# Kernel optimization log

Measured on AMD Instinct MI355X. Metric: run time of the kernel, lower is better.

The kernel has to match this reference:

```python
import jax, jax.numpy as jnp
import numpy as np

N = 50000
E = 800000
D_IN = 128
D_H = 128
D_OUT = 128
G = 64
EPS = 1e-5


def setup_inputs() -> dict:
    key = jax.random.key(0)
    ks = jax.random.split(key, 16)
    s = 0.05
    x = jax.random.normal(ks[0], (N, D_IN), dtype=jnp.float32)
    edge_index = jax.random.randint(ks[1], (2, E), 0, N, dtype=jnp.int64)
    batch = jnp.sort(jax.random.randint(ks[2], (N,), 0, G, dtype=jnp.int64))
    return {
        "x": x,
        "edge_index": edge_index,
        "batch": batch,
        "W1": jax.random.normal(ks[3], (D_IN, D_H), jnp.float32) * s,
        "a_src1": jax.random.normal(ks[4], (D_H,), jnp.float32) * s,
        "a_dst1": jax.random.normal(ks[5], (D_H,), jnp.float32) * s,
        "b1": jnp.zeros((D_H,), jnp.float32),
        "W2": jax.random.normal(ks[6], (D_H, D_H), jnp.float32) * s,
        "a_src2": jax.random.normal(ks[7], (D_H,), jnp.float32) * s,
        "a_dst2": jax.random.normal(ks[8], (D_H,), jnp.float32) * s,
        "b2": jnp.zeros((D_H,), jnp.float32),
        "ln1_g": jnp.ones((D_H,), jnp.float32),
        "ln1_b": jnp.zeros((D_H,), jnp.float32),
        "ln2_g": jnp.ones((D_H,), jnp.float32),
        "ln2_b": jnp.zeros((D_H,), jnp.float32),
        "fc_W": jax.random.normal(ks[9], (D_H, D_OUT), jnp.float32) * s,
        "fc_b": jnp.zeros((D_OUT,), jnp.float32),
        "bn_g": jnp.ones((D_OUT,), jnp.float32),
        "bn_b": jnp.zeros((D_OUT,), jnp.float32),
    }


def gat_conv(x, src, dst, W, a_src, a_dst, b):
    # PyG GATConv, heads=1, concat=False. src=j (message source), dst=i (target).
    h = x @ W                              # [N, C]
    al_s = h @ a_src                       # [N]
    al_d = h @ a_dst                       # [N]
    alpha = jax.nn.leaky_relu(al_s[src] + al_d[dst], 0.2)  # [E']
    m = jax.ops.segment_max(alpha, dst, num_segments=N)    # segment softmax (stable)
    e = jnp.exp(alpha - m[dst])
    z = jax.ops.segment_sum(e, dst, num_segments=N)
    w = e / z[dst]                          # [E']
    out = jax.ops.segment_sum(w[:, None] * h[src], dst, num_segments=N)
    return out + b


def layer_norm(x, g, b):
    mu = jnp.mean(x, axis=-1, keepdims=True)
    var = jnp.mean((x - mu) ** 2, axis=-1, keepdims=True)
    return (x - mu) * jax.lax.rsqrt(var + EPS) * g + b


def reference(x, edge_index, batch, W1, a_src1, a_dst1, b1, W2, a_src2, a_dst2, b2,
              ln1_g, ln1_b, ln2_g, ln2_b, fc_W, fc_b, bn_g, bn_b):
    # add self loops (PyG GATConv default)
    sl = jnp.arange(N, dtype=edge_index.dtype)
    src = jnp.concatenate([edge_index[0], sl])
    dst = jnp.concatenate([edge_index[1], sl])

    h = jax.nn.relu(gat_conv(x, src, dst, W1, a_src1, a_dst1, b1))
    h = layer_norm(h, ln1_g, ln1_b)
    # dropout is identity in eval
    h = gat_conv(h, src, dst, W2, a_src2, a_dst2, b2)
    h = layer_norm(h, ln2_g, ln2_b)
    h = jax.nn.relu(h)

    # global mean pool over graphs
    sums = jax.ops.segment_sum(h, batch, num_segments=G)            # [G, D_H]
    cnts = jax.ops.segment_sum(jnp.ones((N,), h.dtype), batch, num_segments=G)
    pooled = sums / jnp.maximum(cnts, 1.0)[:, None]

    logits = pooled @ fc_W + fc_b                                   # [G, D_OUT]
    # BatchNorm1d (training-mode batch stats, biased variance)
    mu = jnp.mean(logits, axis=0)
    var = jnp.mean((logits - mu) ** 2, axis=0)
    logits = (logits - mu) * jax.lax.rsqrt(var + EPS) * bn_g + bn_b
    return logits
```

## Files before the change

kernel.cpp:

```cpp
#include <hip/hip_runtime.h>
#include <hip/hip_bf16.h>
#include <math.h>

#define N_NODES 50000
#define N_EDGES 800000
#define EN (N_EDGES + N_NODES)
#define D 128
#define G_GRAPHS 64
#define EPS 1e-5f
#define POOL_ROWS_PER_WAVE 64
#define N_TILES 3125
#define LIN_BLOCKS ((N_TILES + 15) / 16)

#define NBUCK 196
#define BCAP 8192
#define EPB 4096
#define BIN_BLOCKS ((EN + EPB - 1) / EPB)

typedef short short8 __attribute__((ext_vector_type(8)));
typedef float f32x4  __attribute__((ext_vector_type(4)));
typedef unsigned short us8 __attribute__((ext_vector_type(8)));

__device__ __forceinline__ float wave_reduce_sum(float v) {
  #pragma unroll
  for (int off = 32; off > 0; off >>= 1) v += __shfl_xor(v, off, 64);
  return v;
}
__device__ __forceinline__ int wave_reduce_sum_i(int v) {
  #pragma unroll
  for (int off = 32; off > 0; off >>= 1) v += __shfl_xor(v, off, 64);
  return v;
}

__device__ __forceinline__ float bf_to_f(unsigned short u) {
  union { unsigned int i; float f; } a;
  a.i = ((unsigned int)u) << 16;
  return a.f;
}
__device__ __forceinline__ unsigned short f_to_bf(float f) {
  union { float f; unsigned int i; } v; v.f = f;
  unsigned int r = v.i + 0x7FFF + ((v.i >> 16) & 1);
  return (unsigned short)(r >> 16);
}


__global__ __launch_bounds__(256) void bin_kernel(
    const int* __restrict__ ei, int* __restrict__ gcnt, uint2* __restrict__ bedges) {
  __shared__ int hist[NBUCK], base[NBUCK], curl[NBUCK];
  int tid = threadIdx.x;
  for (int i = tid; i < NBUCK; i += 256) { hist[i] = 0; curl[i] = 0; }
  __syncthreads();
  int e0 = blockIdx.x * EPB;
  int srcs[16], dsts[16];
  #pragma unroll
  for (int i = 0; i < 16; ++i) {
    int e = e0 + i * 256 + tid;
    int s = -1, d = -1;
    if (e < N_EDGES)   { s = ei[e]; d = ei[N_EDGES + e]; }
    else if (e < EN)   { s = e - N_EDGES; d = s; }
    srcs[i] = s; dsts[i] = d;
    if (d >= 0) atomicAdd(&hist[d >> 8], 1);
  }
  __syncthreads();
  for (int i = tid; i < NBUCK; i += 256)
    base[i] = atomicAdd(&gcnt[i], hist[i]);
  __syncthreads();
  #pragma unroll
  for (int i = 0; i < 16; ++i) {
    int d = dsts[i];
    if (d < 0) continue;
    int b = d >> 8;
    int pos = base[b] + atomicAdd(&curl[b], 1);
    if (pos < BCAP) bedges[(size_t)b * BCAP + pos] = make_uint2((unsigned)srcs[i], (unsigned)d);
  }
}

__global__ __launch_bounds__(256) void bucket_csr_kernel(
    const uint2* __restrict__ bedges, const int* __restrict__ gcnt,
    int* __restrict__ offs, int* __restrict__ esrc, float* __restrict__ sums) {
  __shared__ int hist[256], pex[256], curl[256], scanbuf[256];
  __shared__ int wsum[4];
  int b = blockIdx.x, t = threadIdx.x;
  if (b == 0) {
    for (int i = t; i < G_GRAPHS * D; i += 256) sums[i] = 0.f;
    if (t == 0) offs[N_NODES] = EN;
  }
  int pv = (t < b) ? gcnt[t] : 0;
  int v = wave_reduce_sum_i(pv);
  if ((t & 63) == 0) wsum[t >> 6] = v;
  hist[t] = 0; curl[t] = 0;
  __syncthreads();
  int gb = wsum[0] + wsum[1] + wsum[2] + wsum[3];
  int m = gcnt[b]; if (m > BCAP) m = BCAP;
  int node0 = b << 8;
  const uint2* be = bedges + (size_t)b * BCAP;
  for (int k = t; k < m; k += 256) atomicAdd(&hist[be[k].y & 255], 1);
  __syncthreads();
  int h = hist[t];
  scanbuf[t] = h;
  __syncthreads();
  #pragma unroll
  for (int off = 1; off < 256; off <<= 1) {
    int add = (t >= off) ? scanbuf[t - off] : 0;
    __syncthreads();
    scanbuf[t] += add;
    __syncthreads();
  }
  pex[t] = scanbuf[t] - h;
  int node = node0 + t;
  if (node < N_NODES) offs[node] = gb + pex[t];
  __syncthreads();
  for (int k = t; k < m; k += 256) {
    uint2 e = be[k];
    int n = e.y & 255;
    int r = atomicAdd(&curl[n], 1);
    esrc[gb + pex[n] + r] = (int)e.x;
  }
}


__global__ __launch_bounds__(1024) void linear_mfma_kernel(
    const unsigned short* __restrict__ Xb, const float* __restrict__ Xf,
    const float* __restrict__ W,
    const float* __restrict__ a_s, const float* __restrict__ a_d,
    unsigned short* __restrict__ Hb, float* __restrict__ AS, float* __restrict__ AD) {
  __shared__ unsigned short Wl[D * D];
  int tid = threadIdx.x;
  #pragma unroll
  for (int it = 0; it < 16; ++it) {
    int flat = it * 1024 + tid;
    int r = flat >> 7, col = flat & 127;
    int c = r >> 5, rem = r & 31, quad = rem >> 3, j = rem & 7;
    int t = col >> 4, l = quad * 16 + (col & 15);
    Wl[((t * 4 + c) * 64 + l) * 8 + j] = f_to_bf(W[flat]);
  }
  int lane = tid & 63, wv = tid >> 6;
  int colI = lane & 15, quad = lane >> 4;
  float as_v[8], ad_v[8];
  #pragma unroll
  for (int t = 0; t < 8; ++t) { as_v[t] = a_s[t * 16 + colI]; ad_v[t] = a_d[t * 16 + colI]; }
  __syncthreads();
  int tile = blockIdx.x * 16 + wv;
  if (tile < N_TILES) {
    int row0 = tile * 16;
    short8 afr[4];
    if (Xf) {
      const float* xpf = Xf + (size_t)(row0 + colI) * D + quad * 8;
      #pragma unroll
      for (int c = 0; c < 4; ++c) {
        float4 f0 = *(const float4*)(xpf + c * 32);
        float4 f1 = *(const float4*)(xpf + c * 32 + 4);
        short8 a;
        a[0] = (short)f_to_bf(f0.x); a[1] = (short)f_to_bf(f0.y);
        a[2] = (short)f_to_bf(f0.z); a[3] = (short)f_to_bf(f0.w);
        a[4] = (short)f_to_bf(f1.x); a[5] = (short)f_to_bf(f1.y);
        a[6] = (short)f_to_bf(f1.z); a[7] = (short)f_to_bf(f1.w);
        afr[c] = a;
      }
    } else {
      const unsigned short* xp = Xb + (size_t)(row0 + colI) * D + quad * 8;
      #pragma unroll
      for (int c = 0; c < 4; ++c) afr[c] = *(const short8*)(xp + c * 32);
    }
    f32x4 acc[8];
    #pragma unroll
    for (int t = 0; t < 8; ++t) acc[t] = (f32x4){0.f, 0.f, 0.f, 0.f};
    #pragma unroll
    for (int t = 0; t < 8; ++t) {
      #pragma unroll
      for (int c = 0; c < 4; ++c) {
        short8 bfr = *(const short8*)&Wl[((t * 4 + c) * 64 + lane) * 8];
        acc[t] = __builtin_amdgcn_mfma_f32_16x16x32_bf16(afr[c], bfr, acc[t], 0, 0, 0);
      }
    }
    #pragma unroll
    for (int r = 0; r < 4; ++r) {
      int row = row0 + quad * 4 + r;
      float s = 0.f, dd = 0.f;
      #pragma unroll
      for (int t = 0; t < 8; ++t) {
        float v = acc[t][r];
        Hb[(size_t)row * D + t * 16 + colI] = f_to_bf(v);
        s  = fmaf(v, as_v[t], s);
        dd = fmaf(v, ad_v[t], dd);
      }
      #pragma unroll
      for (int off = 8; off >= 1; off >>= 1) {
        s  += __shfl_xor(s, off, 64);
        dd += __shfl_xor(dd, off, 64);
      }
      if (colI == 0) { AS[row] = s; AD[row] = dd; }
    }
  }
}


__global__ __launch_bounds__(256, 4) void gat_kernel(
    const unsigned short* __restrict__ Hf, const float* __restrict__ AS,
    const float* __restrict__ AD,
    const int* __restrict__ offs, const int* __restrict__ esrc,
    const float* __restrict__ bias, const float* __restrict__ lng, const float* __restrict__ lnb,
    unsigned short* __restrict__ Out, int relu_after) {
  int tid = threadIdx.x;
  int lane = tid & 63;
  int wv = tid >> 6;
  int g4 = lane >> 4, mm = lane & 15;
  int node = blockIdx.x * 16 + wv * 4 + g4;
  if (node >= N_NODES) return;
  int beg = offs[node], end = offs[node + 1];
  float ald = AD[node];
  int base = lane & 48;
  float acc[8];
  #pragma unroll
  for (int d = 0; d < 8; ++d) acc[d] = 0.f;
  float zl = 0.f;
  const unsigned short* hq = Hf + 8 * mm;

  for (int c0 = beg; c0 < end; c0 += 16) {
    int nk = end - c0; if (nk > 16) nk = 16;
    int s_l = 0; float w_l = 0.f;
    if (mm < nk) {
      s_l = esrc[c0 + mm];
      float a = AS[s_l] + ald;
      a = (a > 0.f) ? a : 0.2f * a;
      w_l = __expf(a);
    }
    zl += w_l;
    int   sA = __shfl(s_l, base, 64),     sB = __shfl(s_l, base + 1, 64);
    int   sC = __shfl(s_l, base + 2, 64), sD = __shfl(s_l, base + 3, 64);
    float wA = __shfl(w_l, base, 64),     wB = __shfl(w_l, base + 1, 64);
    float wC = __shfl(w_l, base + 2, 64), wD = __shfl(w_l, base + 3, 64);
    us8 hA = *(const us8*)(hq + (unsigned)sA * D);
    us8 hB = *(const us8*)(hq + (unsigned)sB * D);
    us8 hC = *(const us8*)(hq + (unsigned)sC * D);
    us8 hD = *(const us8*)(hq + (unsigned)sD * D);
    for (int j = 4; j < nk; j += 4) {
      int   sA1 = __shfl(s_l, base + j, 64),     sB1 = __shfl(s_l, base + j + 1, 64);
      int   sC1 = __shfl(s_l, base + j + 2, 64), sD1 = __shfl(s_l, base + j + 3, 64);
      float wA1 = __shfl(w_l, base + j, 64),     wB1 = __shfl(w_l, base + j + 1, 64);
      float wC1 = __shfl(w_l, base + j + 2, 64), wD1 = __shfl(w_l, base + j + 3, 64);
      us8 hA1 = *(const us8*)(hq + (unsigned)sA1 * D);
      us8 hB1 = *(const us8*)(hq + (unsigned)sB1 * D);
      us8 hC1 = *(const us8*)(hq + (unsigned)sC1 * D);
      us8 hD1 = *(const us8*)(hq + (unsigned)sD1 * D);
      #pragma unroll
      for (int d = 0; d < 8; ++d) acc[d] = fmaf(wA, bf_to_f(hA[d]), acc[d]);
      #pragma unroll
      for (int d = 0; d < 8; ++d) acc[d] = fmaf(wB, bf_to_f(hB[d]), acc[d]);
      #pragma unroll
      for (int d = 0; d < 8; ++d) acc[d] = fmaf(wC, bf_to_f(hC[d]), acc[d]);
      #pragma unroll
      for (int d = 0; d < 8; ++d) acc[d] = fmaf(wD, bf_to_f(hD[d]), acc[d]);
      wA = wA1; wB = wB1; wC = wC1; wD = wD1;
      hA = hA1; hB = hB1; hC = hC1; hD = hD1;
    }
    #pragma unroll
    for (int d = 0; d < 8; ++d) acc[d] = fmaf(wA, bf_to_f(hA[d]), acc[d]);
    #pragma unroll
    for (int d = 0; d < 8; ++d) acc[d] = fmaf(wB, bf_to_f(hB[d]), acc[d]);
    #pragma unroll
    for (int d = 0; d < 8; ++d) acc[d] = fmaf(wC, bf_to_f(hC[d]), acc[d]);
    #pragma unroll
    for (int d = 0; d < 8; ++d) acc[d] = fmaf(wD, bf_to_f(hD[d]), acc[d]);
  }

  #pragma unroll
  for (int off = 8; off >= 1; off >>= 1) zl += __shfl_xor(zl, off, 64);
  float inv_z = 1.f / zl;
  const float4* bp = (const float4*)&bias[8 * mm];
  float4 bA4 = bp[0], bB4 = bp[1];
  float bb[8] = {bA4.x, bA4.y, bA4.z, bA4.w, bB4.x, bB4.y, bB4.z, bB4.w};
  float vv[8];
  #pragma unroll
  for (int d = 0; d < 8; ++d) {
    vv[d] = acc[d] * inv_z + bb[d];
    if (!relu_after) vv[d] = fmaxf(vv[d], 0.f);
  }
  float s8 = 0.f, ss = 0.f;
  #pragma unroll
  for (int d = 0; d < 8; ++d) { s8 += vv[d]; ss += vv[d] * vv[d]; }
  #pragma unroll
  for (int off = 8; off >= 1; off >>= 1) {
    s8 += __shfl_xor(s8, off, 64);
    ss += __shfl_xor(ss, off, 64);
  }
  float mean = s8 * (1.f / 128.f);
  float var = ss * (1.f / 128.f) - mean * mean;
  float inv = rsqrtf(var + EPS);
  const float4* gp = (const float4*)&lng[8 * mm];
  const float4* lp = (const float4*)&lnb[8 * mm];
  float4 gA = gp[0], gB = gp[1], lA = lp[0], lB = lp[1];
  float gg[8] = {gA.x, gA.y, gA.z, gA.w, gB.x, gB.y, gB.z, gB.w};
  float ll[8] = {lA.x, lA.y, lA.z, lA.w, lB.x, lB.y, lB.z, lB.w};
  us8 o;
  #pragma unroll
  for (int d = 0; d < 8; ++d) {
    float od = (vv[d] - mean) * inv * gg[d] + ll[d];
    if (relu_after) od = fmaxf(od, 0.f);
    o[d] = f_to_bf(od);
  }
  *(us8*)&Out[(size_t)node * D + 8 * mm] = o;
}


__global__ __launch_bounds__(256) void pool_sum_kernel(
    const unsigned short* __restrict__ Hf, const int* __restrict__ bat,
    float* __restrict__ sums) {
  int lane = threadIdx.x & 63;
  int g4 = lane >> 4, mm = lane & 15;
  int wv = blockIdx.x * 4 + (threadIdx.x >> 6);
  int r0 = wv * POOL_ROWS_PER_WAVE;
  if (r0 >= N_NODES) return;
  int r1 = r0 + POOL_ROWS_PER_WAVE;
  if (r1 > N_NODES) r1 = N_NODES;
  int rs = r0 + g4;
  if (rs >= r1) return;
  float acc[8];
  #pragma unroll
  for (int d = 0; d < 8; ++d) acc[d] = 0.f;
  int g = bat[rs];
  for (int r = rs; r < r1; r += 4) {
    int gr = bat[r];
    if (gr != g) {
      #pragma unroll
      for (int d = 0; d < 8; ++d) atomicAdd(&sums[g * D + 8 * mm + d], acc[d]);
      #pragma unroll
      for (int d = 0; d < 8; ++d) acc[d] = 0.f;
      g = gr;
    }
    us8 hv = *(const us8*)&Hf[(size_t)r * D + 8 * mm];
    #pragma unroll
    for (int d = 0; d < 8; ++d) acc[d] += bf_to_f(hv[d]);
  }
  #pragma unroll
  for (int d = 0; d < 8; ++d) atomicAdd(&sums[g * D + 8 * mm + d], acc[d]);
}

__device__ __forceinline__ int lower_bound_batch(const int* __restrict__ b, int val) {
  int lo = 0, hi = N_NODES;
  while (lo < hi) {
    int mid = (lo + hi) >> 1;
    if (b[mid] < val) lo = mid + 1; else hi = mid;
  }
  return lo;
}

__global__ void fc_kernel(const float* __restrict__ sums, const int* __restrict__ bat,
                          const float* __restrict__ fcW, const float* __restrict__ fcb,
                          float* __restrict__ logits) {
  int g = blockIdx.x;
  int d = threadIdx.x;
  int start = lower_bound_batch(bat, g);
  int end   = lower_bound_batch(bat, g + 1);
  float cnt = (float)(end - start);
  __shared__ float ps[D];
  ps[d] = sums[g * D + d] / fmaxf(cnt, 1.f);
  __syncthreads();
  float o = fcb[d];
  #pragma unroll 8
  for (int k = 0; k < D; ++k) o = fmaf(ps[k], fcW[k * D + d], o);
  logits[g * D + d] = o;
}

__global__ void bn_kernel(const float* __restrict__ logits, const float* __restrict__ g,
                          const float* __restrict__ b, float* __restrict__ out) {
  int d = threadIdx.x;
  float v[G_GRAPHS];
  float mu = 0.f;
  #pragma unroll
  for (int i = 0; i < G_GRAPHS; ++i) { v[i] = logits[i * D + d]; mu += v[i]; }
  mu *= (1.f / G_GRAPHS);
  float var = 0.f;
  #pragma unroll
  for (int i = 0; i < G_GRAPHS; ++i) { float t = v[i] - mu; var += t * t; }
  var *= (1.f / G_GRAPHS);
  float inv = rsqrtf(var + EPS);
  float gg = g[d], bb = b[d];
  #pragma unroll
  for (int i = 0; i < G_GRAPHS; ++i)
    out[i * D + d] = (v[i] - mu) * inv * gg + bb;
}


extern "C" void kernel_launch(void* const* d_in, const int* in_sizes, int n_in,
                              void* d_out, int out_size, void* d_ws, size_t ws_size,
                              hipStream_t stream) {
  const float* x    = (const float*)d_in[0];
  const int*   ei   = (const int*)d_in[1];
  const int*   bat  = (const int*)d_in[2];
  const float* W1   = (const float*)d_in[3];
  const float* as1  = (const float*)d_in[4];
  const float* ad1  = (const float*)d_in[5];
  const float* b1   = (const float*)d_in[6];
  const float* W2   = (const float*)d_in[7];
  const float* as2  = (const float*)d_in[8];
  const float* ad2  = (const float*)d_in[9];
  const float* b2   = (const float*)d_in[10];
  const float* ln1g = (const float*)d_in[11];
  const float* ln1b = (const float*)d_in[12];
  const float* ln2g = (const float*)d_in[13];
  const float* ln2b = (const float*)d_in[14];
  const float* fcW  = (const float*)d_in[15];
  const float* fcb  = (const float*)d_in[16];
  const float* bng  = (const float*)d_in[17];
  const float* bnb  = (const float*)d_in[18];

  char* p = (char*)d_ws;
  auto carve = [&](size_t bytes) { char* r = p; p += (bytes + 255) & ~(size_t)255; return r; };
  int*   offs  = (int*)carve((N_NODES + 1) * sizeof(int));
  int*   gcnt  = (int*)carve(NBUCK * sizeof(int));
  int*   esrc  = (int*)carve((size_t)EN * sizeof(int));
  float* AS    = (float*)carve(N_NODES * sizeof(float));
  float* AD    = (float*)carve(N_NODES * sizeof(float));
  float* LG    = (float*)carve((size_t)G_GRAPHS * D * sizeof(float));
  float* SUMS  = (float*)carve((size_t)G_GRAPHS * D * sizeof(float));
  unsigned short* B1b = (unsigned short*)carve((size_t)N_NODES * D * sizeof(unsigned short));
  unsigned short* B2b = (unsigned short*)carve((size_t)N_NODES * D * sizeof(unsigned short));
  uint2* bedges = (uint2*)B1b;

  const int RB = (N_NODES + 15) / 16;
  const int PB = (N_NODES + 4 * POOL_ROWS_PER_WAVE - 1) / (4 * POOL_ROWS_PER_WAVE);

  hipMemsetAsync(gcnt, 0, NBUCK * sizeof(int), stream);
  bin_kernel<<<BIN_BLOCKS, 256, 0, stream>>>(ei, gcnt, bedges);
  bucket_csr_kernel<<<NBUCK, 256, 0, stream>>>(bedges, gcnt, offs, esrc, SUMS);

  linear_mfma_kernel<<<LIN_BLOCKS, 1024, 0, stream>>>(nullptr, x, W1, as1, ad1, B1b, AS, AD);
  gat_kernel<<<RB, 256, 0, stream>>>(B1b, AS, AD, offs, esrc, b1, ln1g, ln1b, B2b, 0);
  linear_mfma_kernel<<<LIN_BLOCKS, 1024, 0, stream>>>(B2b, nullptr, W2, as2, ad2, B1b, AS, AD);
  gat_kernel<<<RB, 256, 0, stream>>>(B1b, AS, AD, offs, esrc, b2, ln2g, ln2b, B2b, 1);

  pool_sum_kernel<<<PB, 256, 0, stream>>>(B2b, bat, SUMS);
  fc_kernel<<<G_GRAPHS, D, 0, stream>>>(SUMS, bat, fcW, fcb, LG);
  bn_kernel<<<1, D, 0, stream>>>(LG, bng, bnb, (float*)d_out);
}
```

Baseline: 248.5 us.

## Fuse edge binning with first linear layer into one launch

Merges the edge-bucketing kernel and the first MFMA linear kernel into a single launch. The first BIN_BLOCKS blocks bin edges and the remaining blocks compute X·W1 with the attention projections. This removes one kernel launch and lets the two independent stages overlap on the GPU. To avoid a buffer conflict, the bucket scratch moves to B2b and the bucket capacity shrinks to 6144, which still exceeds the average bucket size but leaves less slack for skewed degree distributions. Binning blocks now run 1024 threads with 4 edges each and also reserve the 32KB weight LDS, which may lower occupancy for that part.

```diff
diff --git a/kernel.cpp b/kernel.cpp
--- a/kernel.cpp
+++ b/kernel.cpp
@@ -13,7 +13,7 @@
 #define LIN_BLOCKS ((N_TILES + 15) / 16)
 
 #define NBUCK 196
-#define BCAP 8192
+#define BCAP 6144
 #define EPB 4096
 #define BIN_BLOCKS ((EN + EPB - 1) / EPB)
 
@@ -44,34 +44,102 @@
 }
 
 
-__global__ __launch_bounds__(256) void bin_kernel(
+__global__ __launch_bounds__(1024) void lin1_bin_kernel(
+    const float* __restrict__ Xf, const float* __restrict__ W,
+    const float* __restrict__ a_s, const float* __restrict__ a_d,
+    unsigned short* __restrict__ Hb, float* __restrict__ AS, float* __restrict__ AD,
     const int* __restrict__ ei, int* __restrict__ gcnt, uint2* __restrict__ bedges) {
-  __shared__ int hist[NBUCK], base[NBUCK], curl[NBUCK];
   int tid = threadIdx.x;
-  for (int i = tid; i < NBUCK; i += 256) { hist[i] = 0; curl[i] = 0; }
-  __syncthreads();
-  int e0 = blockIdx.x * EPB;
-  int srcs[16], dsts[16];
-  #pragma unroll
-  for (int i = 0; i < 16; ++i) {
-    int e = e0 + i * 256 + tid;
-    int s = -1, d = -1;
-    if (e < N_EDGES)   { s = ei[e]; d = ei[N_EDGES + e]; }
-    else if (e < EN)   { s = e - N_EDGES; d = s; }
-    srcs[i] = s; dsts[i] = d;
-    if (d >= 0) atomicAdd(&hist[d >> 8], 1);
-  }
-  __syncthreads();
-  for (int i = tid; i < NBUCK; i += 256)
-    base[i] = atomicAdd(&gcnt[i], hist[i]);
-  __syncthreads();
-  #pragma unroll
-  for (int i = 0; i < 16; ++i) {
-    int d = dsts[i];
-    if (d < 0) continue;
-    int b = d >> 8;
-    int pos = base[b] + atomicAdd(&curl[b], 1);
-    if (pos < BCAP) bedges[(size_t)b * BCAP + pos] = make_uint2((unsigned)srcs[i], (unsigned)d);
+  if (blockIdx.x < BIN_BLOCKS) {
+    __shared__ int hist[NBUCK], base[NBUCK], curl[NBUCK];
+    for (int i = tid; i < NBUCK; i += 1024) { hist[i] = 0; curl[i] = 0; }
+    __syncthreads();
+    int e0 = blockIdx.x * EPB;
+    int srcs[4], dsts[4];
+    #pragma unroll
+    for (int i = 0; i < 4; ++i) {
+      int e = e0 + i * 1024 + tid;
+      int s = -1, d = -1;
+      if (e < N_EDGES)   { s = ei[e]; d = ei[N_EDGES + e]; }
+      else if (e < EN)   { s = e - N_EDGES; d = s; }
+      srcs[i] = s; dsts[i] = d;
+      if (d >= 0) atomicAdd(&hist[d >> 8], 1);
+    }
+    __syncthreads();
+    for (int i = tid; i < NBUCK; i += 1024)
+      base[i] = atomicAdd(&gcnt[i], hist[i]);
+    __syncthreads();
+    #pragma unroll
+    for (int i = 0; i < 4; ++i) {
+      int d = dsts[i];
+      if (d < 0) continue;
+      int b = d >> 8;
+      int pos = base[b] + atomicAdd(&curl[b], 1);
+      if (pos < BCAP) bedges[(size_t)b * BCAP + pos] = make_uint2((unsigned)srcs[i], (unsigned)d);
+    }
+    return;
+  }
+  int bb = blockIdx.x - BIN_BLOCKS;
+  __shared__ unsigned short Wl[D * D];
+  #pragma unroll
+  for (int it = 0; it < 16; ++it) {
+    int flat = it * 1024 + tid;
+    int r = flat >> 7, col = flat & 127;
+    int c = r >> 5, rem = r & 31, quad = rem >> 3, j = rem & 7;
+    int t = col >> 4, l = quad * 16 + (col & 15);
+    Wl[((t * 4 + c) * 64 + l) * 8 + j] = f_to_bf(W[flat]);
+  }
+  int lane = tid & 63, wv = tid >> 6;
+  int colI = lane & 15, quad = lane >> 4;
+  float as_v[8], ad_v[8];
+  #pragma unroll
+  for (int t = 0; t < 8; ++t) { as_v[t] = a_s[t * 16 + colI]; ad_v[t] = a_d[t * 16 + colI]; }
+  __syncthreads();
+  int tile = bb * 16 + wv;
+  if (tile < N_TILES) {
+    int row0 = tile * 16;
+    short8 afr[4];
+    const float* xpf = Xf + (size_t)(row0 + colI) * D + quad * 8;
+    #pragma unroll
+    for (int c = 0; c < 4; ++c) {
+      float4 f0 = *(const float4*)(xpf + c * 32);
+      float4 f1 = *(const float4*)(xpf + c * 32 + 4);
+      short8 a;
+      a[0] = (short)f_to_bf(f0.x); a[1] = (short)f_to_bf(f0.y);
+      a[2] = (short)f_to_bf(f0.z); a[3] = (short)f_to_bf(f0.w);
+      a[4] = (short)f_to_bf(f1.x); a[5] = (short)f_to_bf(f1.y);
+      a[6] = (short)f_to_bf(f1.z); a[7] = (short)f_to_bf(f1.w);
+      afr[c] = a;
+    }
+    f32x4 acc[8];
+    #pragma unroll
+    for (int t = 0; t < 8; ++t) acc[t] = (f32x4){0.f, 0.f, 0.f, 0.f};
+    #pragma unroll
+    for (int t = 0; t < 8; ++t) {
+      #pragma unroll
+      for (int c = 0; c < 4; ++c) {
+        short8 bfr = *(const short8*)&Wl[((t * 4 + c) * 64 + lane) * 8];
+        acc[t] = __builtin_amdgcn_mfma_f32_16x16x32_bf16(afr[c], bfr, acc[t], 0, 0, 0);
+      }
+    }
+    #pragma unroll
+    for (int r = 0; r < 4; ++r) {
+      int row = row0 + quad * 4 + r;
+      float s = 0.f, dd = 0.f;
+      #pragma unroll
+      for (int t = 0; t < 8; ++t) {
+        float v = acc[t][r];
+        Hb[(size_t)row * D + t * 16 + colI] = f_to_bf(v);
+        s  = fmaf(v, as_v[t], s);
+        dd = fmaf(v, ad_v[t], dd);
+      }
+      #pragma unroll
+      for (int off = 8; off >= 1; off >>= 1) {
+        s  += __shfl_xor(s, off, 64);
+        dd += __shfl_xor(dd, off, 64);
+      }
+      if (colI == 0) { AS[row] = s; AD[row] = dd; }
+    }
   }
 }
 
@@ -120,7 +188,7 @@
 
 
 __global__ __launch_bounds__(1024) void linear_mfma_kernel(
-    const unsigned short* __restrict__ Xb, const float* __restrict__ Xf,
+    const unsigned short* __restrict__ Xb,
     const float* __restrict__ W,
     const float* __restrict__ a_s, const float* __restrict__ a_d,
     unsigned short* __restrict__ Hb, float* __restrict__ AS, float* __restrict__ AD) {
@@ -144,24 +212,9 @@
   if (tile < N_TILES) {
     int row0 = tile * 16;
     short8 afr[4];
-    if (Xf) {
-      const float* xpf = Xf + (size_t)(row0 + colI) * D + quad * 8;
-      #pragma unroll
-      for (int c = 0; c < 4; ++c) {
-        float4 f0 = *(const float4*)(xpf + c * 32);
-        float4 f1 = *(const float4*)(xpf + c * 32 + 4);
-        short8 a;
-        a[0] = (short)f_to_bf(f0.x); a[1] = (short)f_to_bf(f0.y);
-        a[2] = (short)f_to_bf(f0.z); a[3] = (short)f_to_bf(f0.w);
-        a[4] = (short)f_to_bf(f1.x); a[5] = (short)f_to_bf(f1.y);
-        a[6] = (short)f_to_bf(f1.z); a[7] = (short)f_to_bf(f1.w);
-        afr[c] = a;
-      }
-    } else {
-      const unsigned short* xp = Xb + (size_t)(row0 + colI) * D + quad * 8;
-      #pragma unroll
-      for (int c = 0; c < 4; ++c) afr[c] = *(const short8*)(xp + c * 32);
-    }
+    const unsigned short* xp = Xb + (size_t)(row0 + colI) * D + quad * 8;
+    #pragma unroll
+    for (int c = 0; c < 4; ++c) afr[c] = *(const short8*)(xp + c * 32);
     f32x4 acc[8];
     #pragma unroll
     for (int t = 0; t < 8; ++t) acc[t] = (f32x4){0.f, 0.f, 0.f, 0.f};
@@ -416,18 +469,18 @@
   float* SUMS  = (float*)carve((size_t)G_GRAPHS * D * sizeof(float));
   unsigned short* B1b = (unsigned short*)carve((size_t)N_NODES * D * sizeof(unsigned short));
   unsigned short* B2b = (unsigned short*)carve((size_t)N_NODES * D * sizeof(unsigned short));
-  uint2* bedges = (uint2*)B1b;
+  uint2* bedges = (uint2*)B2b;
 
   const int RB = (N_NODES + 15) / 16;
   const int PB = (N_NODES + 4 * POOL_ROWS_PER_WAVE - 1) / (4 * POOL_ROWS_PER_WAVE);
 
   hipMemsetAsync(gcnt, 0, NBUCK * sizeof(int), stream);
-  bin_kernel<<<BIN_BLOCKS, 256, 0, stream>>>(ei, gcnt, bedges);
+  lin1_bin_kernel<<<BIN_BLOCKS + LIN_BLOCKS, 1024, 0, stream>>>(
+      x, W1, as1, ad1, B1b, AS, AD, ei, gcnt, bedges);
   bucket_csr_kernel<<<NBUCK, 256, 0, stream>>>(bedges, gcnt, offs, esrc, SUMS);
 
-  linear_mfma_kernel<<<LIN_BLOCKS, 1024, 0, stream>>>(nullptr, x, W1, as1, ad1, B1b, AS, AD);
   gat_kernel<<<RB, 256, 0, stream>>>(B1b, AS, AD, offs, esrc, b1, ln1g, ln1b, B2b, 0);
-  linear_mfma_kernel<<<LIN_BLOCKS, 1024, 0, stream>>>(B2b, nullptr, W2, as2, ad2, B1b, AS, AD);
+  linear_mfma_kernel<<<LIN_BLOCKS, 1024, 0, stream>>>(B2b, W2, as2, ad2, B1b, AS, AD);
   gat_kernel<<<RB, 256, 0, stream>>>(B1b, AS, AD, offs, esrc, b2, ln2g, ln2b, B2b, 1);
 
   pool_sum_kernel<<<PB, 256, 0, stream>>>(B2b, bat, SUMS);
```

Result: faster. 240.8 us (-3.1%).
